# Kernel optimization log

Hardware: AMD Instinct MI355X
Metric: run time of the kernel (lower is better)

The kernel has to match this reference:

```python
import jax, jax.numpy as jnp
import numpy as np

N = 100000      # nodes
E = 1600000     # edges (avg degree 16)
F_IN = 500      # input features
D = 64          # hidden dim (args.dim)
C = 40          # classes
EPS = 0.3       # FAConv eps


def setup_inputs() -> dict:
    key = jax.random.key(0)
    ks = jax.random.split(key, 12)
    x = jax.random.normal(ks[0], (N, F_IN), dtype=jnp.float32)
    edge_index = jax.random.randint(ks[1], (2, E), 0, N, dtype=jnp.int32)
    edge_weight_train = jax.random.normal(ks[2], (E,), dtype=jnp.float32)
    t1_w = jax.random.normal(ks[3], (D, F_IN), dtype=jnp.float32) * (1.414 / np.sqrt(F_IN))
    t1_b = jnp.zeros((D,), dtype=jnp.float32)
    att_l1 = jax.random.normal(ks[4], (D,), dtype=jnp.float32) * (1.0 / np.sqrt(D))
    att_r1 = jax.random.normal(ks[5], (D,), dtype=jnp.float32) * (1.0 / np.sqrt(D))
    att_l2 = jax.random.normal(ks[6], (D,), dtype=jnp.float32) * (1.0 / np.sqrt(D))
    att_r2 = jax.random.normal(ks[7], (D,), dtype=jnp.float32) * (1.0 / np.sqrt(D))
    t2_w = jax.random.normal(ks[8], (C, D), dtype=jnp.float32) * (1.414 / np.sqrt(D))
    t2_b = jnp.zeros((C,), dtype=jnp.float32)
    return {"x": x, "edge_index": edge_index, "edge_weight_train": edge_weight_train,
            "t1_w": t1_w, "t1_b": t1_b, "att_l1": att_l1, "att_r1": att_r1,
            "att_l2": att_l2, "att_r2": att_r2, "t2_w": t2_w, "t2_b": t2_b}


def _faconv(h, raw, src, dst, ew, att_l, att_r, n_nodes):
    # FAConv (normalize=False): alpha_e = tanh(a_l.h_src + a_r.h_dst)
    # message m_e = alpha_e * ew_e * h_src; out = eps*raw + scatter_sum_dst(m)
    alpha = jnp.tanh((h @ att_l)[src] + (h @ att_r)[dst])  # [E]
    msg = h[src] * (alpha * ew)[:, None]                   # [E, D]
    agg = jax.ops.segment_sum(msg, dst, num_segments=n_nodes)
    return EPS * raw + agg


def reference(x, edge_index, edge_weight_train, t1_w, t1_b,
              att_l1, att_r1, att_l2, att_r2, t2_w, t2_b):
    n_nodes = x.shape[0]
    # edge masking: |w|>0 drops edges; zeroing the weight is equivalent since
    # the message is multiplied by the edge weight.
    mask = jnp.abs(edge_weight_train) > 0
    ew = jnp.where(mask, jax.nn.sigmoid(edge_weight_train), 0.0)
    src, dst = edge_index[0], edge_index[1]
    # eval mode: dropout disabled
    h = jax.nn.relu(x @ t1_w.T + t1_b)
    raw = h
    h = _faconv(h, raw, src, dst, ew, att_l1, att_r1, n_nodes)
    h = _faconv(h, raw, src, dst, ew, att_l2, att_r2, n_nodes)
    logits = h @ t2_w.T + t2_b
    return jax.nn.log_softmax(logits, axis=1)
```

## Files before the change

kernel.cpp:

```cpp
#include <hip/hip_runtime.h>
#include <hip/hip_bf16.h>

#define NFEAT 500
#define DIM   64
#define NCLS  40
#define EPS_FA 0.3f
#define NPB   32
#define LDSE  1024
#define NCHUNK 256
#define BSH   9

typedef __attribute__((ext_vector_type(8))) __bf16 bf16x8;
typedef __attribute__((ext_vector_type(4))) float  f32x4;

__device__ __forceinline__ float bflo(unsigned int u) {
  return __uint_as_float(u << 16);
}
__device__ __forceinline__ float bfhi(unsigned int u) {
  return __uint_as_float(u & 0xffff0000u);
}
__device__ __forceinline__ float fast_tanh(float x) {
  return 1.f - 2.f / (__expf(2.f * x) + 1.f);
}
__device__ __forceinline__ float sigm(float w) {
  return (__builtin_fabsf(w) > 0.f) ? (1.f / (1.f + __expf(-w))) : 0.f;
}
__device__ __forceinline__ unsigned int packbf(float a, float b) {
  __bf16 x = (__bf16)a, y = (__bf16)b;
  unsigned short ux = *(unsigned short*)&x, uy = *(unsigned short*)&y;
  return (unsigned int)ux | ((unsigned int)uy << 16);
}


__global__ __launch_bounds__(256) void hist2d_kernel(const int* __restrict__ dst,
                                                     int* __restrict__ counts,
                                                     int E, int epc, int nbuk) {
  __shared__ int cnt[256];
  const int c = blockIdx.x;
  for (int i = threadIdx.x; i < nbuk; i += 256) cnt[i] = 0;
  __syncthreads();
  int lo = c * epc, hi = min(E, lo + epc);
  for (int e = lo + threadIdx.x; e < hi; e += 256)
    atomicAdd(&cnt[dst[e] >> BSH], 1);
  __syncthreads();
  for (int i = threadIdx.x; i < nbuk; i += 256)
    counts[i * NCHUNK + c] = cnt[i];
}

__global__ __launch_bounds__(256) void scan_chunks_kernel(int* __restrict__ counts,
                                                          int* __restrict__ buktot) {
  __shared__ int s[256];
  const int b = blockIdx.x, t = threadIdx.x;
  int v = counts[b * NCHUNK + t];
  s[t] = v;
  __syncthreads();
  for (int off = 1; off < 256; off <<= 1) {
    int a = (t >= off) ? s[t - off] : 0;
    __syncthreads();
    s[t] += a;
    __syncthreads();
  }
  counts[b * NCHUNK + t] = s[t] - v;
  if (t == 255) buktot[b] = s[255];
}

__global__ void scan_buckets_kernel(const int* __restrict__ buktot,
                                    int* __restrict__ bukbase, int nbuk) {
  if (blockIdx.x == 0 && threadIdx.x == 0) {
    int run = 0;
    for (int i = 0; i < nbuk; ++i) { bukbase[i] = run; run += buktot[i]; }
    bukbase[nbuk] = run;
  }
}

__global__ __launch_bounds__(256) void scatter_bucket_kernel(const int* __restrict__ src,
                                                             const int* __restrict__ dst,
                                                             const float* __restrict__ ewt,
                                                             const int* __restrict__ counts,
                                                             const int* __restrict__ bukbase,
                                                             int2* __restrict__ tmp,
                                                             int E, int epc, int nbuk) {
  __shared__ int cur[256];
  const int c = blockIdx.x;
  for (int i = threadIdx.x; i < nbuk; i += 256)
    cur[i] = bukbase[i] + counts[i * NCHUNK + c];
  __syncthreads();
  int lo = c * epc, hi = min(E, lo + epc);
  for (int e = lo + threadIdx.x; e < hi; e += 256) {
    int d = dst[e];
    int b = d >> BSH;
    int pos = atomicAdd(&cur[b], 1);
    tmp[pos] = make_int2(src[e] | ((d & 511) << 17), __float_as_int(sigm(ewt[e])));
  }
}

__global__ __launch_bounds__(256) void place_kernel(const int2* __restrict__ tmp,
                                                    const int* __restrict__ bukbase,
                                                    int2* __restrict__ edata,
                                                    int* __restrict__ offs,
                                                    int n, int nbuk) {
  __shared__ int cnt[512];
  __shared__ int loc[512];
  __shared__ int s[256];
  const int b = blockIdx.x, t = threadIdx.x;
  const int base = bukbase[b], end = bukbase[b + 1];
  const int nb0 = b << BSH;
  const int nn = min(512, n - nb0);
  for (int i = t; i < 512; i += 256) cnt[i] = 0;
  __syncthreads();
  for (int i = base + t; i < end; i += 256)
    atomicAdd(&cnt[((unsigned)tmp[i].x) >> 17], 1);
  __syncthreads();
  int a0 = cnt[2 * t], a1 = cnt[2 * t + 1];
  int ps = a0 + a1;
  s[t] = ps;
  __syncthreads();
  for (int off = 1; off < 256; off <<= 1) {
    int ad = (t >= off) ? s[t - off] : 0;
    __syncthreads();
    s[t] += ad;
    __syncthreads();
  }
  int ex = s[t] - ps;
  loc[2 * t] = ex;
  loc[2 * t + 1] = ex + a0;
  __syncthreads();
  for (int j = t; j < nn; j += 256) offs[nb0 + j] = base + loc[j];
  if (b == nbuk - 1 && t == 0) offs[n] = end;
  for (int i = t; i < 512; i += 256) cnt[i] = loc[i];
  __syncthreads();
  for (int i = base + t; i < end; i += 256) {
    int2 r = tmp[i];
    int dl = ((unsigned)r.x) >> 17;
    int pos = atomicAdd(&cnt[dl], 1);
    edata[base + pos] = make_int2(r.x & 0x1FFFF, r.y);
  }
}


__global__ __launch_bounds__(256) void prep_w_kernel(const float* __restrict__ w,
                                                     unsigned short* __restrict__ wh) {
  int i = blockIdx.x * 256 + threadIdx.x;
  int d = i >> 9, k = i & 511;
  float f = (k < NFEAT) ? w[d * NFEAT + k] : 0.f;
  __bf16 b = (__bf16)f;
  wh[i] = *reinterpret_cast<unsigned short*>(&b);
}


__global__ __launch_bounds__(256) void gemm1_kernel(const float* __restrict__ x,
                                                    const unsigned short* __restrict__ whg,
                                                    const float* __restrict__ bias,
                                                    const float* __restrict__ al,
                                                    const float* __restrict__ ar,
                                                    unsigned short* __restrict__ hb,
                                                    float* __restrict__ hl,
                                                    float* __restrict__ hr, int n) {
  __shared__ __bf16 Ah[64][68], Bh[64][68];
  const int tid  = threadIdx.x;
  const int lane = tid & 63;
  const int wv   = tid >> 6;
  const int m0   = blockIdx.x * 64;
  const int r    = lane & 15;
  const int koff = (lane >> 4) * 8;
  const int rowA = wv * 16 + r;

  f32x4 acc[4];
#pragma unroll
  for (int c = 0; c < 4; ++c) acc[c] = (f32x4){0.f, 0.f, 0.f, 0.f};

  for (int kb = 0; kb < 512; kb += 64) {
#pragma unroll
    for (int rr = 0; rr < 4; ++rr) {
      int idx = rr * 256 + tid;
      int m   = idx >> 4;
      int k4  = (idx & 15) << 2;
      int gk  = kb + k4;
      int gm  = m0 + m;
      float4 va = {0.f, 0.f, 0.f, 0.f};
      if (gm < n && gk < NFEAT)
        va = *reinterpret_cast<const float4*>(&x[(size_t)gm * NFEAT + gk]);
      *reinterpret_cast<uint2*>(&Ah[m][k4]) =
          make_uint2(packbf(va.x, va.y), packbf(va.z, va.w));
      *reinterpret_cast<uint2*>(&Bh[m][k4]) =
          *reinterpret_cast<const uint2*>(&whg[m * 512 + gk]);
    }
    __syncthreads();
#pragma unroll
    for (int ks = 0; ks < 2; ++ks) {
      int k0 = ks * 32 + koff;
      bf16x8 a = *reinterpret_cast<const bf16x8*>(&Ah[rowA][k0]);
#pragma unroll
      for (int c = 0; c < 4; ++c) {
        bf16x8 b = *reinterpret_cast<const bf16x8*>(&Bh[c * 16 + r][k0]);
        acc[c] = __builtin_amdgcn_mfma_f32_16x16x32_bf16(a, b, acc[c], 0, 0, 0);
      }
    }
    __syncthreads();
  }

  float rowa[4] = {0.f, 0.f, 0.f, 0.f};
  float rowb[4] = {0.f, 0.f, 0.f, 0.f};
#pragma unroll
  for (int c = 0; c < 4; ++c) {
    int col = c * 16 + r;
    float bv = bias[col], alc = al[col], arc = ar[col];
#pragma unroll
    for (int rr = 0; rr < 4; ++rr) {
      int gmo = m0 + wv * 16 + (lane >> 4) * 4 + rr;
      float v = acc[c][rr] + bv;
      v = v > 0.f ? v : 0.f;
      if (gmo < n) {
        __bf16 vb16 = (__bf16)v;
        hb[(size_t)gmo * DIM + col] = *reinterpret_cast<unsigned short*>(&vb16);
      }
      rowa[rr] = fmaf(v, alc, rowa[rr]);
      rowb[rr] = fmaf(v, arc, rowb[rr]);
    }
  }
#pragma unroll
  for (int rr = 0; rr < 4; ++rr) {
    float a = rowa[rr], b = rowb[rr];
#pragma unroll
    for (int off = 8; off > 0; off >>= 1) {
      a += __shfl_xor(a, off, 64);
      b += __shfl_xor(b, off, 64);
    }
    if (r == 0) {
      int gmo = m0 + wv * 16 + (lane >> 4) * 4 + rr;
      if (gmo < n) { hl[gmo] = a; hr[gmo] = b; }
    }
  }
}


#define EDGE_LOOP(READ_ED)                                                   \
  for (int j = 0; j < mcnt; j += 8) {                                        \
    _Pragma("unroll")                                                        \
    for (int u = 0; u < 8; ++u) {                                            \
      int idx = j + u;                                                       \
      bool valid = idx < cnt;                                                \
      int ci = valid ? s + idx : 0;                                          \
      int2 ed = READ_ED(ci);                                                 \
      int off = valid ? ed.x : 0;                                            \
      float cf = valid ? __int_as_float(ed.y) : 0.f;                         \
      uint4 hv = *reinterpret_cast<const uint4*>((const char*)hb + off + q16);\
      acc0 = fmaf(cf, bflo(hv.x), acc0); acc1 = fmaf(cf, bfhi(hv.x), acc1);  \
      acc2 = fmaf(cf, bflo(hv.y), acc2); acc3 = fmaf(cf, bfhi(hv.y), acc3);  \
      acc4 = fmaf(cf, bflo(hv.z), acc4); acc5 = fmaf(cf, bfhi(hv.z), acc5);  \
      acc6 = fmaf(cf, bflo(hv.w), acc6); acc7 = fmaf(cf, bfhi(hv.w), acc7);  \
    }                                                                        \
  }
#define RD_LDS(ci) eds[ci]
#define RD_GLB(ci) ({ int2 _e = edata[e0 + (ci)];                            \
      float _c = fast_tanh(hlv[_e.x] + hrd) * __int_as_float(_e.y);          \
      make_int2(_e.x * 128, __float_as_int(_c)); })

#define STAGE_EDGES(HLV, HRL)                                                \
  for (int i = tid; i < nE && i < LDSE; i += 256) {                          \
    int2 e = edata[e0 + i];                                                  \
    int key = e0 + i;                                                        \
    int nd = 0;                                                              \
    _Pragma("unroll")                                                        \
    for (int st = 16; st >= 1; st >>= 1)                                     \
      if (offs_l[nd + st] <= key) nd += st;                                  \
    float c = fast_tanh(HLV[e.x] + HRL[nd]) * __int_as_float(e.y);           \
    eds[i] = make_int2(e.x * 128, __float_as_int(c));                        \
  }

#define AGG_PROLOGUE()                                                       \
  const int tid  = threadIdx.x;                                              \
  const int lane = tid & 63;                                                 \
  const int wv   = tid >> 6;                                                 \
  const int g    = lane >> 3;                        \
  const int q    = lane & 7;                                  \
  const int q16  = q << 4;                                                   \
  const int n0   = blockIdx.x * NPB;                                         \
  if (tid <= NPB) {                                                          \
    int nd = n0 + tid;                                                       \
    offs_l[tid] = offs[nd < n ? nd : n];                                     \
  }                                                                          \
  if (tid < NPB) {                                                           \
    int nd = n0 + tid;                                                       \
    hr_l[tid] = nd < n ? hrv[nd] : 0.f;                                      \
  }

#define AGG_BODY()                                                           \
  const int e0 = offs_l[0];                                                  \
  const int nE = offs_l[NPB] - e0;                                           \
  STAGE_EDGES(hlv, hr_l)                                                     \
  __syncthreads();                                                           \
  const int node = n0 + wv * 8 + g;                                          \
  int s = 0, cnt = 0;                                                        \
  float hrd = 0.f;                                                           \
  if (node < n) {                                                            \
    s = offs_l[wv * 8 + g] - e0;                                             \
    cnt = offs_l[wv * 8 + g + 1] - e0 - s;                                   \
    hrd = hr_l[wv * 8 + g];                                                  \
  }                                                                          \
  int mcnt = cnt;                                                            \
  mcnt = max(mcnt, __shfl_xor(mcnt, 8, 64));                                 \
  mcnt = max(mcnt, __shfl_xor(mcnt, 16, 64));                                \
  mcnt = max(mcnt, __shfl_xor(mcnt, 32, 64));                                \
  float acc0 = 0.f, acc1 = 0.f, acc2 = 0.f, acc3 = 0.f;                      \
  float acc4 = 0.f, acc5 = 0.f, acc6 = 0.f, acc7 = 0.f;                      \
  if (nE <= LDSE) { EDGE_LOOP(RD_LDS) } else { EDGE_LOOP(RD_GLB) }


__global__ __launch_bounds__(256) void agg1_kernel(const unsigned short* __restrict__ hb,
                                                   const int2* __restrict__ edata,
                                                   const int* __restrict__ offs,
                                                   const float* __restrict__ hlv,
                                                   const float* __restrict__ hrv,
                                                   const float* __restrict__ al2,
                                                   const float* __restrict__ ar2,
                                                   unsigned short* __restrict__ h1b,
                                                   float* __restrict__ hl2,
                                                   float* __restrict__ hr2, int n) {
  __shared__ int2 eds[LDSE];
  __shared__ int offs_l[NPB + 1];
  __shared__ float hr_l[NPB];
  AGG_PROLOGUE()
  __syncthreads();
  AGG_BODY()

  if (node < n) {
    uint4 rv = *reinterpret_cast<const uint4*>((const char*)hb + (size_t)node * 128 + q16);
    float v0 = fmaf(EPS_FA, bflo(rv.x), acc0);
    float v1 = fmaf(EPS_FA, bfhi(rv.x), acc1);
    float v2 = fmaf(EPS_FA, bflo(rv.y), acc2);
    float v3 = fmaf(EPS_FA, bfhi(rv.y), acc3);
    float v4 = fmaf(EPS_FA, bflo(rv.z), acc4);
    float v5 = fmaf(EPS_FA, bfhi(rv.z), acc5);
    float v6 = fmaf(EPS_FA, bflo(rv.w), acc6);
    float v7 = fmaf(EPS_FA, bfhi(rv.w), acc7);
    uint4 pk = make_uint4(packbf(v0, v1), packbf(v2, v3), packbf(v4, v5), packbf(v6, v7));
    *reinterpret_cast<uint4*>((char*)h1b + (size_t)node * 128 + q16) = pk;
    const float4 ala = *reinterpret_cast<const float4*>(al2 + q * 8);
    const float4 alb = *reinterpret_cast<const float4*>(al2 + q * 8 + 4);
    const float4 ara = *reinterpret_cast<const float4*>(ar2 + q * 8);
    const float4 arb = *reinterpret_cast<const float4*>(ar2 + q * 8 + 4);
    float a = v0 * ala.x + v1 * ala.y + v2 * ala.z + v3 * ala.w
            + v4 * alb.x + v5 * alb.y + v6 * alb.z + v7 * alb.w;
    float b = v0 * ara.x + v1 * ara.y + v2 * ara.z + v3 * ara.w
            + v4 * arb.x + v5 * arb.y + v6 * arb.z + v7 * arb.w;
#pragma unroll
    for (int off = 4; off > 0; off >>= 1) {
      a += __shfl_xor(a, off, 64);
      b += __shfl_xor(b, off, 64);
    }
    if (q == 0) { hl2[node] = a; hr2[node] = b; }
  }
}


__global__ __launch_bounds__(256) void agg_cls_kernel(const unsigned short* __restrict__ hb,
                                                      const unsigned short* __restrict__ rawb,
                                                      const int2* __restrict__ edata,
                                                      const int* __restrict__ offs,
                                                      const float* __restrict__ hlv,
                                                      const float* __restrict__ hrv,
                                                      const float* __restrict__ t2w,
                                                      const float* __restrict__ t2b,
                                                      float* __restrict__ out, int n) {
  __shared__ int2 eds[LDSE];
  __shared__ int offs_l[NPB + 1];
  __shared__ float hr_l[NPB];
  __shared__ float t2s[DIM * NCLS];
  __shared__ float rowbuf[NPB][DIM];
  AGG_PROLOGUE()
  for (int i = tid; i < DIM * NCLS; i += 256) {
    int k = i / NCLS, cls = i - k * NCLS;
    t2s[i] = t2w[cls * DIM + k];
  }
  __syncthreads();
  AGG_BODY()

  if (node >= n) return;
  const int nl = wv * 8 + g;
  {
    uint4 rv = *reinterpret_cast<const uint4*>((const char*)rawb + (size_t)node * 128 + q16);
    float4 va, vb;
    va.x = fmaf(EPS_FA, bflo(rv.x), acc0);
    va.y = fmaf(EPS_FA, bfhi(rv.x), acc1);
    va.z = fmaf(EPS_FA, bflo(rv.y), acc2);
    va.w = fmaf(EPS_FA, bfhi(rv.y), acc3);
    vb.x = fmaf(EPS_FA, bflo(rv.z), acc4);
    vb.y = fmaf(EPS_FA, bfhi(rv.z), acc5);
    vb.z = fmaf(EPS_FA, bflo(rv.w), acc6);
    vb.w = fmaf(EPS_FA, bfhi(rv.w), acc7);
    *reinterpret_cast<float4*>(&rowbuf[nl][q * 8])     = va;
    *reinterpret_cast<float4*>(&rowbuf[nl][q * 8 + 4]) = vb;
  }
  float lg[5];
#pragma unroll
  for (int j = 0; j < 5; ++j) lg[j] = t2b[q + 8 * j];
#pragma unroll
  for (int k = 0; k < DIM; ++k) {
    float rr = rowbuf[nl][k];
#pragma unroll
    for (int j = 0; j < 5; ++j)
      lg[j] = fmaf(rr, t2s[k * NCLS + q + 8 * j], lg[j]);
  }
  float mx = lg[0];
#pragma unroll
  for (int j = 1; j < 5; ++j) mx = fmaxf(mx, lg[j]);
#pragma unroll
  for (int off = 4; off > 0; off >>= 1) mx = fmaxf(mx, __shfl_xor(mx, off, 64));
  float ssum = 0.f;
#pragma unroll
  for (int j = 0; j < 5; ++j) ssum += __expf(lg[j] - mx);
#pragma unroll
  for (int off = 4; off > 0; off >>= 1) ssum += __shfl_xor(ssum, off, 64);
  float lse = mx + __logf(ssum);
  float* op = out + (size_t)node * NCLS;
#pragma unroll
  for (int j = 0; j < 5; ++j) op[q + 8 * j] = lg[j] - lse;
}


extern "C" void kernel_launch(void* const* d_in, const int* in_sizes, int n_in,
                              void* d_out, int out_size, void* d_ws, size_t ws_size,
                              hipStream_t stream) {
  const float* x   = (const float*)d_in[0];
  const int*   ei  = (const int*)d_in[1];
  const float* ewt = (const float*)d_in[2];
  const float* t1w = (const float*)d_in[3];
  const float* t1b = (const float*)d_in[4];
  const float* al1 = (const float*)d_in[5];
  const float* ar1 = (const float*)d_in[6];
  const float* al2 = (const float*)d_in[7];
  const float* ar2 = (const float*)d_in[8];
  const float* t2w = (const float*)d_in[9];
  const float* t2b = (const float*)d_in[10];
  float* out = (float*)d_out;

  const int n = in_sizes[0] / NFEAT;
  const int E = in_sizes[2];
  const int* srcp = ei;
  const int* dstp = ei + E;

  char* p = (char*)d_ws;
  auto alloc = [&](size_t bytes) {
    char* q = p;
    p += (bytes + 255) & ~(size_t)255;
    return q;
  };
  unsigned short* h0b = (unsigned short*)alloc((size_t)n * DIM * 2);
  unsigned short* h1b = (unsigned short*)alloc((size_t)n * DIM * 2);
  float* hl    = (float*)alloc((size_t)n * 4);
  float* hr    = (float*)alloc((size_t)n * 4);
  float* hl2   = (float*)alloc((size_t)n * 4);
  float* hr2   = (float*)alloc((size_t)n * 4);
  int*   offs  = (int*)alloc((size_t)(n + 1) * 4);
  int2*  edata = (int2*)alloc((size_t)E * 8);
  int2*  tmp   = (int2*)alloc((size_t)E * 8);
  unsigned short* whg = (unsigned short*)alloc((size_t)DIM * 512 * 2);
  int*   counts = (int*)alloc((size_t)256 * NCHUNK * 4);
  int*   buktot = (int*)alloc(256 * 4);
  int*   bukbase= (int*)alloc(257 * 4);

  const int nbuk = (n + 511) >> BSH;
  const int epc  = (E + NCHUNK - 1) / NCHUNK;

  hist2d_kernel<<<NCHUNK, 256, 0, stream>>>(dstp, counts, E, epc, nbuk);
  scan_chunks_kernel<<<nbuk, 256, 0, stream>>>(counts, buktot);
  scan_buckets_kernel<<<1, 64, 0, stream>>>(buktot, bukbase, nbuk);
  scatter_bucket_kernel<<<NCHUNK, 256, 0, stream>>>(srcp, dstp, ewt, counts, bukbase,
                                                    tmp, E, epc, nbuk);
  place_kernel<<<nbuk, 256, 0, stream>>>(tmp, bukbase, edata, offs, n, nbuk);

  prep_w_kernel<<<(DIM * 512) / 256, 256, 0, stream>>>(t1w, whg);
  gemm1_kernel<<<(n + 63) / 64, 256, 0, stream>>>(x, whg, t1b, al1, ar1,
                                                  h0b, hl, hr, n);

  const int ab = (n + NPB - 1) / NPB;
  agg1_kernel<<<ab, 256, 0, stream>>>(h0b, edata, offs, hl, hr, al2, ar2, h1b, hl2, hr2, n);
  agg_cls_kernel<<<ab, 256, 0, stream>>>(h1b, h0b, edata, offs, hl2, hr2, t2w, t2b, out, n);
}
```

Before: 226.8 us.

## Sort nodes by degree per block and enlarge GEMM row tile to 128

In both aggregation kernels, each block ranks its 32 nodes by edge count and maps them to 8-lane groups in descending-degree order. Groups in the same wave then have similar degrees, so the shared loop bound (the max count across the wave) wastes fewer iterations. Separately, the first GEMM now handles 128 rows per block, with each wave computing two 16-row MFMA tiles. This reuses every loaded weight tile twice and halves the number of blocks. The costs are a small serial ranking step, an extra shared permutation array, and more accumulator registers in the GEMM.

```diff
diff --git a/kernel.cpp b/kernel.cpp
--- a/kernel.cpp
+++ b/kernel.cpp
@@ -156,22 +156,23 @@
                                                     unsigned short* __restrict__ hb,
                                                     float* __restrict__ hl,
                                                     float* __restrict__ hr, int n) {
-  __shared__ __bf16 Ah[64][68], Bh[64][68];
+  __shared__ __bf16 Ah[128][68], Bh[64][68];
   const int tid  = threadIdx.x;
   const int lane = tid & 63;
   const int wv   = tid >> 6;
-  const int m0   = blockIdx.x * 64;
+  const int m0   = blockIdx.x * 128;
   const int r    = lane & 15;
   const int koff = (lane >> 4) * 8;
-  const int rowA = wv * 16 + r;
-
-  f32x4 acc[4];
-#pragma unroll
-  for (int c = 0; c < 4; ++c) acc[c] = (f32x4){0.f, 0.f, 0.f, 0.f};
+
+  f32x4 acc[2][4];
+#pragma unroll
+  for (int rg = 0; rg < 2; ++rg)
+#pragma unroll
+    for (int c = 0; c < 4; ++c) acc[rg][c] = (f32x4){0.f, 0.f, 0.f, 0.f};
 
   for (int kb = 0; kb < 512; kb += 64) {
 #pragma unroll
-    for (int rr = 0; rr < 4; ++rr) {
+    for (int rr = 0; rr < 8; ++rr) {
       int idx = rr * 256 + tid;
       int m   = idx >> 4;
       int k4  = (idx & 15) << 2;
@@ -182,53 +183,64 @@
         va = *reinterpret_cast<const float4*>(&x[(size_t)gm * NFEAT + gk]);
       *reinterpret_cast<uint2*>(&Ah[m][k4]) =
           make_uint2(packbf(va.x, va.y), packbf(va.z, va.w));
+    }
+#pragma unroll
+    for (int rr = 0; rr < 4; ++rr) {
+      int idx = rr * 256 + tid;
+      int m   = idx >> 4;
+      int k4  = (idx & 15) << 2;
       *reinterpret_cast<uint2*>(&Bh[m][k4]) =
-          *reinterpret_cast<const uint2*>(&whg[m * 512 + gk]);
+          *reinterpret_cast<const uint2*>(&whg[m * 512 + kb + k4]);
     }
     __syncthreads();
 #pragma unroll
     for (int ks = 0; ks < 2; ++ks) {
       int k0 = ks * 32 + koff;
-      bf16x8 a = *reinterpret_cast<const bf16x8*>(&Ah[rowA][k0]);
+      bf16x8 a0 = *reinterpret_cast<const bf16x8*>(&Ah[wv * 32 + r][k0]);
+      bf16x8 a1 = *reinterpret_cast<const bf16x8*>(&Ah[wv * 32 + 16 + r][k0]);
 #pragma unroll
       for (int c = 0; c < 4; ++c) {
         bf16x8 b = *reinterpret_cast<const bf16x8*>(&Bh[c * 16 + r][k0]);
-        acc[c] = __builtin_amdgcn_mfma_f32_16x16x32_bf16(a, b, acc[c], 0, 0, 0);
+        acc[0][c] = __builtin_amdgcn_mfma_f32_16x16x32_bf16(a0, b, acc[0][c], 0, 0, 0);
+        acc[1][c] = __builtin_amdgcn_mfma_f32_16x16x32_bf16(a1, b, acc[1][c], 0, 0, 0);
       }
     }
     __syncthreads();
   }
 
-  float rowa[4] = {0.f, 0.f, 0.f, 0.f};
-  float rowb[4] = {0.f, 0.f, 0.f, 0.f};
-#pragma unroll
-  for (int c = 0; c < 4; ++c) {
-    int col = c * 16 + r;
-    float bv = bias[col], alc = al[col], arc = ar[col];
+#pragma unroll
+  for (int rg = 0; rg < 2; ++rg) {
+    float rowa[4] = {0.f, 0.f, 0.f, 0.f};
+    float rowb[4] = {0.f, 0.f, 0.f, 0.f};
+#pragma unroll
+    for (int c = 0; c < 4; ++c) {
+      int col = c * 16 + r;
+      float bv = bias[col], alc = al[col], arc = ar[col];
+#pragma unroll
+      for (int rr = 0; rr < 4; ++rr) {
+        int gmo = m0 + wv * 32 + rg * 16 + (lane >> 4) * 4 + rr;
+        float v = acc[rg][c][rr] + bv;
+        v = v > 0.f ? v : 0.f;
+        if (gmo < n) {
+          __bf16 vb16 = (__bf16)v;
+          hb[(size_t)gmo * DIM + col] = *reinterpret_cast<unsigned short*>(&vb16);
+        }
+        rowa[rr] = fmaf(v, alc, rowa[rr]);
+        rowb[rr] = fmaf(v, arc, rowb[rr]);
+      }
+    }
 #pragma unroll
     for (int rr = 0; rr < 4; ++rr) {
-      int gmo = m0 + wv * 16 + (lane >> 4) * 4 + rr;
-      float v = acc[c][rr] + bv;
-      v = v > 0.f ? v : 0.f;
-      if (gmo < n) {
-        __bf16 vb16 = (__bf16)v;
-        hb[(size_t)gmo * DIM + col] = *reinterpret_cast<unsigned short*>(&vb16);
+      float a = rowa[rr], b = rowb[rr];
+#pragma unroll
+      for (int off = 8; off > 0; off >>= 1) {
+        a += __shfl_xor(a, off, 64);
+        b += __shfl_xor(b, off, 64);
       }
-      rowa[rr] = fmaf(v, alc, rowa[rr]);
-      rowb[rr] = fmaf(v, arc, rowb[rr]);
-    }
-  }
-#pragma unroll
-  for (int rr = 0; rr < 4; ++rr) {
-    float a = rowa[rr], b = rowb[rr];
-#pragma unroll
-    for (int off = 8; off > 0; off >>= 1) {
-      a += __shfl_xor(a, off, 64);
-      b += __shfl_xor(b, off, 64);
-    }
-    if (r == 0) {
-      int gmo = m0 + wv * 16 + (lane >> 4) * 4 + rr;
-      if (gmo < n) { hl[gmo] = a; hr[gmo] = b; }
+      if (r == 0) {
+        int gmo = m0 + wv * 32 + rg * 16 + (lane >> 4) * 4 + rr;
+        if (gmo < n) { hl[gmo] = a; hr[gmo] = b; }
+      }
     }
   }
 }
@@ -272,7 +284,7 @@
   const int tid  = threadIdx.x;                                              \
   const int lane = tid & 63;                                                 \
   const int wv   = tid >> 6;                                                 \
-  const int g    = lane >> 3;                        \
+  const int g    = lane >> 3;                                \
   const int q    = lane & 7;                                  \
   const int q16  = q << 4;                                                   \
   const int n0   = blockIdx.x * NPB;                                         \
@@ -285,18 +297,31 @@
     hr_l[tid] = nd < n ? hrv[nd] : 0.f;                                      \
   }
 
+#define AGG_RANK()                                                           \
+  if (tid < NPB) {                                                           \
+    int c_i = offs_l[tid + 1] - offs_l[tid];                                 \
+    int rank = 0;                                                            \
+    _Pragma("unroll")                                                        \
+    for (int j = 0; j < NPB; ++j) {                                          \
+      int c_j = offs_l[j + 1] - offs_l[j];                                   \
+      rank += (c_j > c_i) || (c_j == c_i && j < tid);                        \
+    }                                                                        \
+    perm[rank] = (unsigned char)tid;                                         \
+  }
+
 #define AGG_BODY()                                                           \
   const int e0 = offs_l[0];                                                  \
   const int nE = offs_l[NPB] - e0;                                           \
   STAGE_EDGES(hlv, hr_l)                                                     \
   __syncthreads();                                                           \
-  const int node = n0 + wv * 8 + g;                                          \
+  const int pn = perm[wv * 8 + g];                                           \
+  const int node = n0 + pn;                                                  \
   int s = 0, cnt = 0;                                                        \
   float hrd = 0.f;                                                           \
   if (node < n) {                                                            \
-    s = offs_l[wv * 8 + g] - e0;                                             \
-    cnt = offs_l[wv * 8 + g + 1] - e0 - s;                                   \
-    hrd = hr_l[wv * 8 + g];                                                  \
+    s = offs_l[pn] - e0;                                                     \
+    cnt = offs_l[pn + 1] - offs_l[pn];                                       \
+    hrd = hr_l[pn];                                                          \
   }                                                                          \
   int mcnt = cnt;                                                            \
   mcnt = max(mcnt, __shfl_xor(mcnt, 8, 64));                                 \
@@ -320,8 +345,10 @@
   __shared__ int2 eds[LDSE];
   __shared__ int offs_l[NPB + 1];
   __shared__ float hr_l[NPB];
+  __shared__ unsigned char perm[NPB];
   AGG_PROLOGUE()
   __syncthreads();
+  AGG_RANK()
   AGG_BODY()
 
   if (node < n) {
@@ -366,6 +393,7 @@
   __shared__ int2 eds[LDSE];
   __shared__ int offs_l[NPB + 1];
   __shared__ float hr_l[NPB];
+  __shared__ unsigned char perm[NPB];
   __shared__ float t2s[DIM * NCLS];
   __shared__ float rowbuf[NPB][DIM];
   AGG_PROLOGUE()
@@ -374,6 +402,7 @@
     t2s[i] = t2w[cls * DIM + k];
   }
   __syncthreads();
+  AGG_RANK()
   AGG_BODY()
 
   if (node >= n) return;
@@ -471,8 +500,8 @@
   place_kernel<<<nbuk, 256, 0, stream>>>(tmp, bukbase, edata, offs, n, nbuk);
 
   prep_w_kernel<<<(DIM * 512) / 256, 256, 0, stream>>>(t1w, whg);
-  gemm1_kernel<<<(n + 63) / 64, 256, 0, stream>>>(x, whg, t1b, al1, ar1,
-                                                  h0b, hl, hr, n);
+  gemm1_kernel<<<(n + 127) / 128, 256, 0, stream>>>(x, whg, t1b, al1, ar1,
+                                                    h0b, hl, hr, n);
 
   const int ab = (n + NPB - 1) / NPB;
   agg1_kernel<<<ab, 256, 0, stream>>>(h0b, edata, offs, hl, hr, al2, ar2, h1b, hl2, hr2, n);
```

Result: slower. 239.1 us (+5.4%).
